# Kernel optimization log

Measured on AMD Instinct MI355X. Metric: run time of the kernel, lower is better.

The kernel has to match this reference:

```python
import math
import jax, jax.numpy as jnp
import numpy as np

D_MODEL, D_K, D_V = 512, 64, 64
B, S = 4, 4096

def setup_inputs() -> dict:
    key = jax.random.key(0)
    ks = jax.random.split(key, 7)
    scale_in = 1.0 / math.sqrt(D_MODEL)
    return {
        "x": jax.random.normal(ks[0], (B, S, D_MODEL), dtype=jnp.float32),
        "wq": jax.random.normal(ks[1], (D_MODEL, D_K), dtype=jnp.float32) * scale_in,
        "bq": jax.random.normal(ks[2], (D_K,), dtype=jnp.float32) * 0.02,
        "wk": jax.random.normal(ks[3], (D_MODEL, D_K), dtype=jnp.float32) * scale_in,
        "bk": jax.random.normal(ks[4], (D_K,), dtype=jnp.float32) * 0.02,
        "wv": jax.random.normal(ks[5], (D_MODEL, D_V), dtype=jnp.float32) * scale_in,
        "bv": jax.random.normal(ks[6], (D_V,), dtype=jnp.float32) * 0.02,
    }

def reference(x, wq, bq, wk, bk, wv, bv):
    # q,k: [B,S,Dk]; v: [B,S,Dv]
    q = jnp.einsum("bsd,dk->bsk", x, wq) + bq
    k = jnp.einsum("bsd,dk->bsk", x, wk) + bk
    v = jnp.einsum("bsd,dv->bsv", x, wv) + bv
    inv_sqrt_dk = 1.0 / math.sqrt(D_K)
    scores = jnp.einsum("bqk,bsk->bqs", q, k) * inv_sqrt_dk  # [B,S,S]
    probs = jax.nn.softmax(scores, axis=2)
    return jnp.einsum("bqs,bsv->bqv", probs, v)  # [B,S,Dv]
```

## Files before the change

### kernel.cpp

```cpp
#include <hip/hip_runtime.h>
#include <hip/hip_bf16.h>
#include <cstddef>
#include <cstdint>

#define DM 512
#define DK 64
#define BB 4
#define S4 4096
#define NR (BB*S4)
#define KVB 64
#define QBLOCK 128
#define LP 72

typedef float   f32x16 __attribute__((ext_vector_type(16)));
typedef short   bf16x8 __attribute__((ext_vector_type(8)));

#define QSCALE 0.18033688011112042f

__device__ __forceinline__ ushort bf16bits(float f) {
    __hip_bfloat16 h = __float2bfloat16(f);
    return *reinterpret_cast<ushort*>(&h);
}

__device__ __forceinline__ uint32_t cvtpk(float a, float b) {
    uint32_t d;
    asm("v_cvt_pk_bf16_f32 %0, %1, %2" : "=v"(d) : "v"(a), "v"(b));
    return d;
}

__device__ __forceinline__ void permswap(uint32_t& a, uint32_t& b) {
    asm("v_permlane32_swap_b32 %0, %1" : "+v"(a), "+v"(b));
}

__global__ __launch_bounds__(256) void prep_w(
    const float* __restrict__ wq, const float* __restrict__ wk,
    const float* __restrict__ wv,
    ushort* __restrict__ Wfh, ushort* __restrict__ Wfl)
{
    const int id = blockIdx.x * 256 + threadIdx.x;
    const int c  = id >> 9, k = id & 511;
    const float* src = (c < 64) ? wq : (c < 128) ? wk : wv;
    const float wval = src[k * DK + (c & 63)];
    const ushort h  = bf16bits(wval);
    __hip_bfloat16 hh = *reinterpret_cast<const __hip_bfloat16*>(&h);
    const ushort l  = bf16bits(wval - __bfloat162float(hh));
    const int ko = k >> 6, ks = (k >> 4) & 3, kh = (k >> 3) & 1, e = k & 7;
    const size_t idx = ((size_t)((ko * 4 + ks) * 2 + kh) * 192 + c) * 8 + e;
    Wfh[idx] = h;
    Wfl[idx] = l;
}

__global__ __launch_bounds__(256, 3) void qkv_mfma(
    const float* __restrict__ x,
    const ushort* __restrict__ Wfh, const ushort* __restrict__ Wfl,
    const float* __restrict__ bq, const float* __restrict__ bk,
    const float* __restrict__ bv,
    ushort* __restrict__ Qb, ushort* __restrict__ Kb, ushort* __restrict__ Vb)
{
    __shared__ ushort Xh[64 * 64];
    __shared__ ushort Xl[64 * 64];

    const int tid  = threadIdx.x;
    const int w    = tid >> 6;
    const int lane = tid & 63;
    const int hi   = lane >> 5;
    const int q5   = lane & 31;
    const int wr   = w >> 1, wc = w & 1;
    const size_t row0 = (size_t)blockIdx.x * 64;
    const int cidx = blockIdx.y * 2 + wc;
    const int arow = wr * 32 + q5;

    float4 xr[4];
    uint2  ch[4], cl[4];

    auto gx = [&](int ko) {
        #pragma unroll
        for (int i = 0; i < 4; ++i) {
            const int idx = i * 256 + tid, r = idx >> 4, kc = idx & 15;
            xr[i] = *(const float4*)&x[(row0 + r) * DM + ko * 64 + kc * 4];
        }
    };
    auto cvt_all = [&]() {
        #pragma unroll
        for (int i = 0; i < 4; ++i) {
            const uint32_t h01 = cvtpk(xr[i].x, xr[i].y);
            const uint32_t h23 = cvtpk(xr[i].z, xr[i].w);
            const float hf0 = __uint_as_float(h01 << 16);
            const float hf1 = __uint_as_float(h01 & 0xFFFF0000u);
            const float hf2 = __uint_as_float(h23 << 16);
            const float hf3 = __uint_as_float(h23 & 0xFFFF0000u);
            ch[i] = (uint2){h01, h23};
            cl[i] = (uint2){cvtpk(xr[i].x - hf0, xr[i].y - hf1),
                            cvtpk(xr[i].z - hf2, xr[i].w - hf3)};
        }
    };

    f32x16 acc = {};

    gx(0);
    cvt_all();

    for (int ko = 0; ko < 8; ++ko) {
        __syncthreads();
        #pragma unroll
        for (int i = 0; i < 4; ++i) {
            const int idx = i * 256 + tid, r = idx >> 4, kc = idx & 15;
            const int byte = (r * 128 + kc * 8) ^ ((r & 7) << 4);
            *reinterpret_cast<uint2*>((char*)Xh + byte) = ch[i];
            *reinterpret_cast<uint2*>((char*)Xl + byte) = cl[i];
        }
        __syncthreads();
        if (ko < 7) gx(ko + 1);

        #pragma unroll
        for (int ks = 0; ks < 4; ++ks) {
            const int abyte = (arow * 128 + ks * 32 + hi * 16) ^ ((arow & 7) << 4);
            const bf16x8 ah = *reinterpret_cast<const bf16x8*>((char*)Xh + abyte);
            const bf16x8 al = *reinterpret_cast<const bf16x8*>((char*)Xl + abyte);
            const int seg = (ko * 4 + ks) * 2 + hi;
            const size_t wb = ((size_t)seg * 192 + cidx * 32 + q5) * 8;
            const bf16x8 bh = *reinterpret_cast<const bf16x8*>(Wfh + wb);
            const bf16x8 bl = *reinterpret_cast<const bf16x8*>(Wfl + wb);
            acc = __builtin_amdgcn_mfma_f32_32x32x16_bf16(ah, bh, acc, 0, 0, 0);
            acc = __builtin_amdgcn_mfma_f32_32x32x16_bf16(al, bh, acc, 0, 0, 0);
            acc = __builtin_amdgcn_mfma_f32_32x32x16_bf16(ah, bl, acc, 0, 0, 0);
        }
        if (ko < 7) cvt_all();
    }

    const float* bp[3] = {bq, bk, bv};
    ushort*      op[3] = {Qb, Kb, Vb};
    const int mi = cidx >> 1, half = cidx & 1;
    const float bias = bp[mi][half * 32 + q5];
    #pragma unroll
    for (int r = 0; r < 16; ++r) {
        const int rr = (r & 3) + 8 * (r >> 2) + 4 * hi;
        const size_t grow = row0 + wr * 32 + rr;
        float v = acc[r] + bias;
        if (mi == 0) v *= QSCALE;
        op[mi][grow * DK + half * 32 + q5] = bf16bits(v);
    }
}

__global__ __launch_bounds__(256) void transpose_v(
    const ushort* __restrict__ V, ushort* __restrict__ Vt)
{
    __shared__ ushort t[64 * 72];
    const int tid = threadIdx.x;
    const int s0  = blockIdx.x * 64;
    const int b   = blockIdx.y;
    const int sr  = tid >> 2, c = tid & 3;

    const uint4* src = reinterpret_cast<const uint4*>(
        V + ((size_t)b * S4 + s0 + sr) * DK + c * 16);
    uint4 v0 = src[0], v1 = src[1];
    *reinterpret_cast<uint4*>(&t[sr * 72 + c * 16])     = v0;
    *reinterpret_cast<uint4*>(&t[sr * 72 + c * 16 + 8]) = v1;
    __syncthreads();

    const int dv = tid >> 2;
    alignas(16) ushort o[16];
    #pragma unroll
    for (int i = 0; i < 16; ++i) o[i] = t[(c * 16 + i) * 72 + dv];
    uint4* dst = reinterpret_cast<uint4*>(
        Vt + ((size_t)b * DK + dv) * S4 + s0 + c * 16);
    dst[0] = *reinterpret_cast<const uint4*>(&o[0]);
    dst[1] = *reinterpret_cast<const uint4*>(&o[8]);
}

__global__ __launch_bounds__(256, 4) void attn_mfma(
    const ushort* __restrict__ Qb, const ushort* __restrict__ Kb,
    const ushort* __restrict__ Vt,
    float* __restrict__ Opart, float* __restrict__ Lpart,
    float* __restrict__ out, int sigma)
{
    __shared__ ushort Ks[2][64 * LP];
    __shared__ ushort Vs[2][64 * LP];

    const int tid  = threadIdx.x;
    const int w    = tid >> 6;
    const int lane = tid & 63;
    const int hi   = lane >> 5;
    const int q5   = lane & 31;
    const int b    = blockIdx.y, ci = blockIdx.z;
    const int klen = S4 / sigma, kv0 = ci * klen;
    const int qrow = blockIdx.x * QBLOCK + w * 32 + q5;

    const int c0 = tid, c1 = tid + 256;
    const int r0 = c0 >> 3, cc0 = c0 & 7;
    const int r1 = c1 >> 3, cc1 = c1 & 7;

    bf16x8 qf[4];
    {
        const ushort* qp = Qb + ((size_t)b * S4 + qrow) * DK;
        #pragma unroll
        for (int s = 0; s < 4; ++s)
            qf[s] = *reinterpret_cast<const bf16x8*>(qp + s * 16 + hi * 8);
    }

    bf16x8 onesv;
    #pragma unroll
    for (int i = 0; i < 8; ++i) onesv[i] = (short)0x3F80;

    f32x16 oacc0 = {}, oacc1 = {}, lacc = {};

    uint4 kreg0, kreg1, vreg0, vreg1;
    auto gload = [&](int t) {
        const ushort* gK = Kb + ((size_t)b * S4 + kv0 + t * KVB) * DK;
        const ushort* gV = Vt + (size_t)b * DK * S4 + (kv0 + t * KVB);
        kreg0 = *reinterpret_cast<const uint4*>(gK + r0 * DK + cc0 * 8);
        kreg1 = *reinterpret_cast<const uint4*>(gK + r1 * DK + cc1 * 8);
        vreg0 = *reinterpret_cast<const uint4*>(gV + (size_t)r0 * S4 + cc0 * 8);
        vreg1 = *reinterpret_cast<const uint4*>(gV + (size_t)r1 * S4 + cc1 * 8);
    };
    auto stage = [&](int buf) {
        *reinterpret_cast<uint4*>(&Ks[buf][r0 * LP + cc0 * 8]) = kreg0;
        *reinterpret_cast<uint4*>(&Ks[buf][r1 * LP + cc1 * 8]) = kreg1;
        *reinterpret_cast<uint4*>(&Vs[buf][r0 * LP + cc0 * 8]) = vreg0;
        *reinterpret_cast<uint4*>(&Vs[buf][r1 * LP + cc1 * 8]) = vreg1;
    };

    const int nt = klen / KVB;
    gload(0);
    stage(0);
    if (nt > 1) gload(1);
    __syncthreads();

    for (int t = 0; t < nt; ++t) {
        const int cur = t & 1;
        if (t + 1 < nt) {
            stage(cur ^ 1);
            if (t + 2 < nt) gload(t + 2);
        }
        const ushort* Kbuf = &Ks[cur][0];
        const ushort* Vbuf = &Vs[cur][0];

        #pragma unroll
        for (int sub = 0; sub < 2; ++sub) {
            const int kvr = sub * 32 + q5;
            bf16x8 kf[4];
            #pragma unroll
            for (int s = 0; s < 4; ++s)
                kf[s] = *reinterpret_cast<const bf16x8*>(
                    &Kbuf[kvr * LP + (2 * s + hi) * 8]);
            f32x16 sacc = {};
            #pragma unroll
            for (int s = 0; s < 4; ++s)
                sacc = __builtin_amdgcn_mfma_f32_32x32x16_bf16(
                    kf[s], qf[s], sacc, 0, 0, 0);

            float p[16];
            #pragma unroll
            for (int r = 0; r < 16; ++r) p[r] = exp2f(sacc[r]);

            uint32_t wd[8];
            #pragma unroll
            for (int g = 0; g < 4; ++g) {
                wd[2 * g]     = cvtpk(p[4 * g],     p[4 * g + 1]);
                wd[2 * g + 1] = cvtpk(p[4 * g + 2], p[4 * g + 3]);
            }
            permswap(wd[0], wd[2]);  permswap(wd[1], wd[3]);
            permswap(wd[4], wd[6]);  permswap(wd[5], wd[7]);
            union { uint32_t u[4]; bf16x8 v; } pa0, pa1;
            pa0.u[0] = wd[0]; pa0.u[1] = wd[1]; pa0.u[2] = wd[2]; pa0.u[3] = wd[3];
            pa1.u[0] = wd[4]; pa1.u[1] = wd[5]; pa1.u[2] = wd[6]; pa1.u[3] = wd[7];

            lacc = __builtin_amdgcn_mfma_f32_32x32x16_bf16(pa0.v, onesv, lacc, 0, 0, 0);
            lacc = __builtin_amdgcn_mfma_f32_32x32x16_bf16(pa1.v, onesv, lacc, 0, 0, 0);

            #pragma unroll
            for (int h = 0; h < 2; ++h) {
                const int dv = h * 32 + q5;
                #pragma unroll
                for (int tt = 0; tt < 2; ++tt) {
                    const bf16x8 vf = *reinterpret_cast<const bf16x8*>(
                        &Vbuf[dv * LP + (sub * 4 + tt * 2 + hi) * 8]);
                    if (h == 0)
                        oacc0 = __builtin_amdgcn_mfma_f32_32x32x16_bf16(
                            tt == 0 ? pa0.v : pa1.v, vf, oacc0, 0, 0, 0);
                    else
                        oacc1 = __builtin_amdgcn_mfma_f32_32x32x16_bf16(
                            tt == 0 ? pa0.v : pa1.v, vf, oacc1, 0, 0, 0);
                }
            }
        }
        __syncthreads();
    }

    if (sigma == 1) {
        #pragma unroll
        for (int r = 0; r < 16; ++r) {
            const int qq = (r & 3) + 8 * (r >> 2) + 4 * hi;
            const float inv = 1.0f / lacc[r];
            const size_t row = (size_t)b * S4 + blockIdx.x * QBLOCK + w * 32 + qq;
            out[row * DK + q5]      = oacc0[r] * inv;
            out[row * DK + 32 + q5] = oacc1[r] * inv;
        }
    } else {
        if (q5 == 0) {
            #pragma unroll
            for (int r = 0; r < 16; ++r) {
                const int qq = (r & 3) + 8 * (r >> 2) + 4 * hi;
                const size_t row = (size_t)b * S4 + blockIdx.x * QBLOCK + w * 32 + qq;
                Lpart[(size_t)ci * NR + row] = lacc[r];
            }
        }
        #pragma unroll
        for (int r = 0; r < 16; ++r) {
            const int qq = (r & 3) + 8 * (r >> 2) + 4 * hi;
            const size_t row = (size_t)b * S4 + blockIdx.x * QBLOCK + w * 32 + qq;
            float* op = Opart + ((size_t)ci * NR + row) * DK;
            op[q5]      = oacc0[r];
            op[32 + q5] = oacc1[r];
        }
    }
}

__global__ __launch_bounds__(256) void attn_reduce(
    const float* __restrict__ Opart, const float* __restrict__ Lpart,
    float* __restrict__ out, int sigma)
{
    const int e4  = blockIdx.x * 256 + threadIdx.x;
    const int row = e4 >> 4;
    const int d4  = e4 & 15;

    float L = 0.0f;
    float4 O = {0.0f, 0.0f, 0.0f, 0.0f};
    for (int i = 0; i < sigma; ++i) {
        L += Lpart[(size_t)i * NR + row];
        const float4 o = *reinterpret_cast<const float4*>(
            Opart + (((size_t)i * NR + row) << 6) + d4 * 4);
        O.x += o.x; O.y += o.y; O.z += o.z; O.w += o.w;
    }
    const float inv = 1.0f / L;
    float4 res = {O.x * inv, O.y * inv, O.z * inv, O.w * inv};
    *reinterpret_cast<float4*>(out + ((size_t)row << 6) + d4 * 4) = res;
}

extern "C" void kernel_launch(void* const* d_in, const int* in_sizes, int n_in,
                              void* d_out, int out_size, void* d_ws, size_t ws_size,
                              hipStream_t stream)
{
    const float* x  = (const float*)d_in[0];
    const float* wq = (const float*)d_in[1];
    const float* bq = (const float*)d_in[2];
    const float* wk = (const float*)d_in[3];
    const float* bk = (const float*)d_in[4];
    const float* wv = (const float*)d_in[5];
    const float* bv = (const float*)d_in[6];

    char* ws = (char*)d_ws;
    const size_t MB2  = (size_t)NR * DK * 2;
    const size_t WTSZ = (size_t)192 * DM * 2;

    ushort* Qb  = (ushort*)(ws);
    ushort* Kb  = (ushort*)(ws + MB2);
    ushort* Vb  = (ushort*)(ws + 2 * MB2);
    ushort* Vt  = (ushort*)(ws + 3 * MB2);
    ushort* Wfh = (ushort*)(ws + 4 * MB2);
    ushort* Wfl = (ushort*)(ws + 4 * MB2 + WTSZ);

    const size_t POFF = 4 * MB2 + 2 * WTSZ;

    int sigma = 1;
    const int cand[2] = {4, 2};
    for (int i = 0; i < 2; ++i) {
        const int s = cand[i];
        const size_t need = POFF + (size_t)s * ((size_t)NR * DK * 4 + (size_t)NR * 4);
        if (need <= ws_size) { sigma = s; break; }
    }

    float* Opart = (float*)(ws + POFF);
    float* Lpart = (float*)(ws + POFF + (size_t)sigma * NR * DK * 4);

    prep_w<<<384, 256, 0, stream>>>(wq, wk, wv, Wfh, Wfl);
    qkv_mfma<<<dim3(NR / 64, 3), 256, 0, stream>>>(x, Wfh, Wfl, bq, bk, bv,
                                                   Qb, Kb, Vb);
    transpose_v<<<dim3(S4 / 64, BB), 256, 0, stream>>>(Vb, Vt);

    dim3 grid(S4 / QBLOCK, BB, sigma);
    attn_mfma<<<grid, 256, 0, stream>>>(Qb, Kb, Vt, Opart, Lpart,
                                        (float*)d_out, sigma);

    if (sigma > 1)
        attn_reduce<<<(NR * DK) / 1024, 256, 0, stream>>>(Opart, Lpart,
                                                          (float*)d_out, sigma);
}
```

Measured before the change: 77.15 us.

## Fuse V transpose into QKV projection epilogue and double attention KV tile

The V projection blocks now transpose their output tile through shared memory and write V directly in transposed layout. This removes the separate transpose kernel and its extra global read/write pass. The attention kernel also processes 128 keys per tile instead of 64, with larger padded K/V shared buffers and launch bounds lowered to 2 blocks per CU. That halves the loop iterations and barriers, but uses more LDS and registers and may reduce occupancy.

Result: slower. 93.52 us (+21.2%).

```diff
diff --git a/kernel.cpp b/kernel.cpp
--- a/kernel.cpp
+++ b/kernel.cpp
@@ -8,9 +8,10 @@
 #define BB 4
 #define S4 4096
 #define NR (BB*S4)
-#define KVB 64
+#define KVB 128
 #define QBLOCK 128
-#define LP 72
+#define KP 72
+#define VP 136
 
 typedef float   f32x16 __attribute__((ext_vector_type(16)));
 typedef short   bf16x8 __attribute__((ext_vector_type(8)));
@@ -55,10 +56,11 @@
     const ushort* __restrict__ Wfh, const ushort* __restrict__ Wfl,
     const float* __restrict__ bq, const float* __restrict__ bk,
     const float* __restrict__ bv,
-    ushort* __restrict__ Qb, ushort* __restrict__ Kb, ushort* __restrict__ Vb)
-{
-    __shared__ ushort Xh[64 * 64];
-    __shared__ ushort Xl[64 * 64];
+    ushort* __restrict__ Qb, ushort* __restrict__ Kb, ushort* __restrict__ Vt)
+{
+    __shared__ ushort smem[2][64 * 64];
+    ushort* Xh = &smem[0][0];
+    ushort* Xl = &smem[1][0];
 
     const int tid  = threadIdx.x;
     const int w    = tid >> 6;
@@ -128,54 +130,48 @@
         if (ko < 7) cvt_all();
     }
 
+    const int mi = cidx >> 1, half = cidx & 1;
     const float* bp[3] = {bq, bk, bv};
-    ushort*      op[3] = {Qb, Kb, Vb};
-    const int mi = cidx >> 1, half = cidx & 1;
     const float bias = bp[mi][half * 32 + q5];
-    #pragma unroll
-    for (int r = 0; r < 16; ++r) {
-        const int rr = (r & 3) + 8 * (r >> 2) + 4 * hi;
-        const size_t grow = row0 + wr * 32 + rr;
-        float v = acc[r] + bias;
-        if (mi == 0) v *= QSCALE;
-        op[mi][grow * DK + half * 32 + q5] = bf16bits(v);
-    }
-}
-
-__global__ __launch_bounds__(256) void transpose_v(
-    const ushort* __restrict__ V, ushort* __restrict__ Vt)
-{
-    __shared__ ushort t[64 * 72];
-    const int tid = threadIdx.x;
-    const int s0  = blockIdx.x * 64;
-    const int b   = blockIdx.y;
-    const int sr  = tid >> 2, c = tid & 3;
-
-    const uint4* src = reinterpret_cast<const uint4*>(
-        V + ((size_t)b * S4 + s0 + sr) * DK + c * 16);
-    uint4 v0 = src[0], v1 = src[1];
-    *reinterpret_cast<uint4*>(&t[sr * 72 + c * 16])     = v0;
-    *reinterpret_cast<uint4*>(&t[sr * 72 + c * 16 + 8]) = v1;
-    __syncthreads();
-
-    const int dv = tid >> 2;
-    alignas(16) ushort o[16];
-    #pragma unroll
-    for (int i = 0; i < 16; ++i) o[i] = t[(c * 16 + i) * 72 + dv];
-    uint4* dst = reinterpret_cast<uint4*>(
-        Vt + ((size_t)b * DK + dv) * S4 + s0 + c * 16);
-    dst[0] = *reinterpret_cast<const uint4*>(&o[0]);
-    dst[1] = *reinterpret_cast<const uint4*>(&o[8]);
-}
-
-__global__ __launch_bounds__(256, 4) void attn_mfma(
+
+    if (blockIdx.y == 2) {
+        __syncthreads();
+        ushort* vt = &smem[0][0];
+        #pragma unroll
+        for (int r = 0; r < 16; ++r) {
+            const int rr = (r & 3) + 8 * (r >> 2) + 4 * hi;
+            vt[(half * 32 + q5) * 72 + wr * 32 + rr] = bf16bits(acc[r] + bias);
+        }
+        __syncthreads();
+        const int dv = tid >> 2, sc = tid & 3;
+        const int bb = (int)(row0 >> 12);
+        const int sb = (int)(row0 & (S4 - 1));
+        const ushort* src = vt + dv * 72 + sc * 16;
+        uint4* dst = reinterpret_cast<uint4*>(
+            Vt + ((size_t)bb * DK + dv) * S4 + sb + sc * 16);
+        dst[0] = *reinterpret_cast<const uint4*>(src);
+        dst[1] = *reinterpret_cast<const uint4*>(src + 8);
+    } else {
+        ushort* op = (mi == 0) ? Qb : Kb;
+        #pragma unroll
+        for (int r = 0; r < 16; ++r) {
+            const int rr = (r & 3) + 8 * (r >> 2) + 4 * hi;
+            const size_t grow = row0 + wr * 32 + rr;
+            float v = acc[r] + bias;
+            if (mi == 0) v *= QSCALE;
+            op[grow * DK + half * 32 + q5] = bf16bits(v);
+        }
+    }
+}
+
+__global__ __launch_bounds__(256, 2) void attn_mfma(
     const ushort* __restrict__ Qb, const ushort* __restrict__ Kb,
     const ushort* __restrict__ Vt,
     float* __restrict__ Opart, float* __restrict__ Lpart,
     float* __restrict__ out, int sigma)
 {
-    __shared__ ushort Ks[2][64 * LP];
-    __shared__ ushort Vs[2][64 * LP];
+    __shared__ ushort Ks[2][KVB * KP];
+    __shared__ ushort Vs[2][64 * VP];
 
     const int tid  = threadIdx.x;
     const int w    = tid >> 6;
@@ -186,9 +182,13 @@
     const int klen = S4 / sigma, kv0 = ci * klen;
     const int qrow = blockIdx.x * QBLOCK + w * 32 + q5;
 
-    const int c0 = tid, c1 = tid + 256;
-    const int r0 = c0 >> 3, cc0 = c0 & 7;
-    const int r1 = c1 >> 3, cc1 = c1 & 7;
+    int rK[4], cK[4], rV[4], cV[4];
+    #pragma unroll
+    for (int i = 0; i < 4; ++i) {
+        const int c = i * 256 + tid;
+        rK[i] = c >> 3;  cK[i] = c & 7;
+        rV[i] = c >> 4;  cV[i] = c & 15;
+    }
 
     bf16x8 qf[4];
     {
@@ -204,20 +204,22 @@
 
     f32x16 oacc0 = {}, oacc1 = {}, lacc = {};
 
-    uint4 kreg0, kreg1, vreg0, vreg1;
+    uint4 kreg[4], vreg[4];
     auto gload = [&](int t) {
         const ushort* gK = Kb + ((size_t)b * S4 + kv0 + t * KVB) * DK;
         const ushort* gV = Vt + (size_t)b * DK * S4 + (kv0 + t * KVB);
-        kreg0 = *reinterpret_cast<const uint4*>(gK + r0 * DK + cc0 * 8);
-        kreg1 = *reinterpret_cast<const uint4*>(gK + r1 * DK + cc1 * 8);
-        vreg0 = *reinterpret_cast<const uint4*>(gV + (size_t)r0 * S4 + cc0 * 8);
-        vreg1 = *reinterpret_cast<const uint4*>(gV + (size_t)r1 * S4 + cc1 * 8);
+        #pragma unroll
+        for (int i = 0; i < 4; ++i) {
+            kreg[i] = *reinterpret_cast<const uint4*>(gK + rK[i] * DK + cK[i] * 8);
+            vreg[i] = *reinterpret_cast<const uint4*>(gV + (size_t)rV[i] * S4 + cV[i] * 8);
+        }
     };
     auto stage = [&](int buf) {
-        *reinterpret_cast<uint4*>(&Ks[buf][r0 * LP + cc0 * 8]) = kreg0;
-        *reinterpret_cast<uint4*>(&Ks[buf][r1 * LP + cc1 * 8]) = kreg1;
-        *reinterpret_cast<uint4*>(&Vs[buf][r0 * LP + cc0 * 8]) = vreg0;
-        *reinterpret_cast<uint4*>(&Vs[buf][r1 * LP + cc1 * 8]) = vreg1;
+        #pragma unroll
+        for (int i = 0; i < 4; ++i) {
+            *reinterpret_cast<uint4*>(&Ks[buf][rK[i] * KP + cK[i] * 8]) = kreg[i];
+            *reinterpret_cast<uint4*>(&Vs[buf][rV[i] * VP + cV[i] * 8]) = vreg[i];
+        }
     };
 
     const int nt = klen / KVB;
@@ -236,13 +238,13 @@
         const ushort* Vbuf = &Vs[cur][0];
 
         #pragma unroll
-        for (int sub = 0; sub < 2; ++sub) {
+        for (int sub = 0; sub < 4; ++sub) {
             const int kvr = sub * 32 + q5;
             bf16x8 kf[4];
             #pragma unroll
             for (int s = 0; s < 4; ++s)
                 kf[s] = *reinterpret_cast<const bf16x8*>(
-                    &Kbuf[kvr * LP + (2 * s + hi) * 8]);
+                    &Kbuf[kvr * KP + (2 * s + hi) * 8]);
             f32x16 sacc = {};
             #pragma unroll
             for (int s = 0; s < 4; ++s)
@@ -274,7 +276,7 @@
                 #pragma unroll
                 for (int tt = 0; tt < 2; ++tt) {
                     const bf16x8 vf = *reinterpret_cast<const bf16x8*>(
-                        &Vbuf[dv * LP + (sub * 4 + tt * 2 + hi) * 8]);
+                        &Vbuf[dv * VP + (sub * 4 + tt * 2 + hi) * 8]);
                     if (h == 0)
                         oacc0 = __builtin_amdgcn_mfma_f32_32x32x16_bf16(
                             tt == 0 ? pa0.v : pa1.v, vf, oacc0, 0, 0, 0);
@@ -355,12 +357,11 @@
 
     ushort* Qb  = (ushort*)(ws);
     ushort* Kb  = (ushort*)(ws + MB2);
-    ushort* Vb  = (ushort*)(ws + 2 * MB2);
-    ushort* Vt  = (ushort*)(ws + 3 * MB2);
-    ushort* Wfh = (ushort*)(ws + 4 * MB2);
-    ushort* Wfl = (ushort*)(ws + 4 * MB2 + WTSZ);
-
-    const size_t POFF = 4 * MB2 + 2 * WTSZ;
+    ushort* Vt  = (ushort*)(ws + 2 * MB2);
+    ushort* Wfh = (ushort*)(ws + 3 * MB2);
+    ushort* Wfl = (ushort*)(ws + 3 * MB2 + WTSZ);
+
+    const size_t POFF = 3 * MB2 + 2 * WTSZ;
 
     int sigma = 1;
     const int cand[2] = {4, 2};
@@ -375,8 +376,7 @@
 
     prep_w<<<384, 256, 0, stream>>>(wq, wk, wv, Wfh, Wfl);
     qkv_mfma<<<dim3(NR / 64, 3), 256, 0, stream>>>(x, Wfh, Wfl, bq, bk, bv,
-                                                   Qb, Kb, Vb);
-    transpose_v<<<dim3(S4 / 64, BB), 256, 0, stream>>>(Vb, Vt);
+                                                   Qb, Kb, Vt);
 
     dim3 grid(S4 / QBLOCK, BB, sigma);
     attn_mfma<<<grid, 256, 0, stream>>>(Qb, Kb, Vt, Opart, Lpart,
```
